# Kernel optimization log

Measured on AMD Instinct MI355X. Metric: run time of the kernel, lower is better.

The kernel has to match this reference:

```python
import jax, jax.numpy as jnp
import numpy as np

B, N, F, A, E, D, V, L = 128, 36, 2048, 1024, 1024, 1024, 10000, 20


def setup_inputs() -> dict:
    key = jax.random.key(0)
    ks = jax.random.split(key, 24)
    s = 0.02
    image_features = jax.random.normal(ks[0], (B, N, F), jnp.float32)
    encoded_captions = jax.random.randint(ks[1], (B, L), 0, V, jnp.int32)
    caption_lengths = jax.random.randint(ks[2], (B, 1), 5, L + 1, jnp.int32)
    caption_lengths = caption_lengths.at[0, 0].set(L)  # ensure max decode len = L-1
    p = lambda k, shape: jax.random.normal(k, shape, jnp.float32) * s
    return {
        "image_features": image_features,
        "encoded_captions": encoded_captions,
        "caption_lengths": caption_lengths,
        "emb": jax.random.uniform(ks[3], (V, E), jnp.float32, -0.1, 0.1),
        "W1_ih": p(ks[4], (4 * D, E + F + D)),
        "W1_hh": p(ks[5], (4 * D, D)),
        "b1_ih": jnp.zeros((4 * D,), jnp.float32),
        "b1_hh": jnp.zeros((4 * D,), jnp.float32),
        "W2_ih": p(ks[6], (4 * D, F + D)),
        "W2_hh": p(ks[7], (4 * D, D)),
        "b2_ih": jnp.zeros((4 * D,), jnp.float32),
        "b2_hh": jnp.zeros((4 * D,), jnp.float32),
        "Wf": p(ks[8], (A, F)),
        "bf": jnp.zeros((A,), jnp.float32),
        "Wd": p(ks[9], (A, D)),
        "bd": jnp.zeros((A,), jnp.float32),
        "Wa": p(ks[10], (1, A)),
        "ba": jnp.zeros((1,), jnp.float32),
        "Wfc": jax.random.uniform(ks[11], (V, D), jnp.float32, -0.1, 0.1),
        "bfc": jnp.zeros((V,), jnp.float32),
    }


def _lstm_cell(x, h, c, Wih, Whh, bih, bhh):
    g = x @ Wih.T + bih + h @ Whh.T + bhh
    i, f, gg, o = jnp.split(g, 4, axis=-1)
    c2 = jax.nn.sigmoid(f) * c + jax.nn.sigmoid(i) * jnp.tanh(gg)
    h2 = jax.nn.sigmoid(o) * jnp.tanh(c2)
    return h2, c2


def reference(image_features, encoded_captions, caption_lengths, emb,
              W1_ih, W1_hh, b1_ih, b1_hh, W2_ih, W2_hh, b2_ih, b2_hh,
              Wf, bf, Wd, bd, Wa, ba, Wfc, bfc):
    lengths = caption_lengths[:, 0]
    sort_ind = jnp.argsort(-lengths)  # descending, as in torch sort
    feats = image_features[sort_ind]            # [B,N,F]
    caps = encoded_captions[sort_ind]           # [B,L]
    dec_len = lengths[sort_ind] - 1             # [B]
    feats_mean = feats.mean(axis=1)             # [B,F]
    embs = emb[caps]                            # [B,L,E]
    att1 = feats @ Wf.T + bf                    # [B,N,A] (constant per step)
    T = caps.shape[1] - 1
    d = feats.dtype
    h1 = jnp.zeros((caps.shape[0], W1_hh.shape[1]), d)
    c1, h2, c2 = h1, h1, h1

    def step(carry, xs):
        h1, c1, h2, c2 = carry
        emb_t, t = xs
        active = (t < dec_len)[:, None].astype(d)  # ragged batch mask
        x1 = jnp.concatenate([h2, feats_mean, emb_t], axis=1)
        nh1, nc1 = _lstm_cell(x1, h1, c1, W1_ih, W1_hh, b1_ih, b1_hh)
        h1 = active * nh1 + (1.0 - active) * h1
        c1 = active * nc1 + (1.0 - active) * c1
        # additive attention (dropout is identity at eval)
        att2 = h1 @ Wd.T + bd                   # [B,A]
        e = (jax.nn.relu(att1 + att2[:, None, :]) @ Wa.T + ba)[..., 0]  # [B,N]
        alpha = jax.nn.softmax(e, axis=1)
        awe = jnp.einsum('bnf,bn->bf', feats, alpha)
        x2 = jnp.concatenate([awe, h1], axis=1)
        nh2, nc2 = _lstm_cell(x2, h2, c2, W2_ih, W2_hh, b2_ih, b2_hh)
        h2 = active * nh2 + (1.0 - active) * h2
        c2 = active * nc2 + (1.0 - active) * c2
        preds = (h2 @ Wfc.T + bfc) * active     # zeros past decode_length
        return (h1, c1, h2, c2), preds

    xs = (jnp.swapaxes(embs[:, :T, :], 0, 1), jnp.arange(T))
    _, preds = jax.lax.scan(step, (h1, c1, h2, c2), xs)
    return jnp.transpose(preds, (1, 0, 2))      # [B,T,V]
```

## Files before the change

kernel.cpp:

```cpp
#include <hip/hip_runtime.h>
#include <hip/hip_bf16.h>
#include <math.h>

#define B   128
#define NN  36
#define FF  2048
#define AA  1024
#define EE  1024
#define DD  1024
#define VV  10000
#define LL  20
#define TT  19

typedef __attribute__((ext_vector_type(8))) short short8;
typedef __attribute__((ext_vector_type(4))) float floatx4;

__global__ __launch_bounds__(B) void sort_kernel(const int* __restrict__ cap_len,
                                                 int* __restrict__ sort_ind,
                                                 int* __restrict__ dec_len) {
    __shared__ int lsh[B];
    int i = threadIdx.x;
    lsh[i] = cap_len[i];
    __syncthreads();
    int li = lsh[i];
    int rank = 0;
    for (int j = 0; j < B; ++j) {
        int lj = lsh[j];
        rank += (lj > li) || (lj == li && j < i);
    }
    sort_ind[rank] = i;
    dec_len[rank]  = li - 1;
}

__global__ void convert_kernel(const float* __restrict__ src,
                               __hip_bfloat16* __restrict__ dst, int n) {
    int i = blockIdx.x * 256 + threadIdx.x;
    if (i < n) dst[i] = __float2bfloat16(src[i]);
}

__global__ void pack_w1dyn_kernel(const float* __restrict__ Wih,
                                  const float* __restrict__ Whh,
                                  __hip_bfloat16* __restrict__ dst) {
    int i = blockIdx.x * 256 + threadIdx.x;
    int n = i >> 11, k = i & 2047;
    float v = (k < 1024) ? Wih[(size_t)n * 4096 + k] : Whh[(size_t)n * 1024 + (k - 1024)];
    dst[i] = __float2bfloat16(v);
}

__global__ void pack_w1fm_kernel(const float* __restrict__ Wih,
                                 __hip_bfloat16* __restrict__ dst) {
    int i = blockIdx.x * 256 + threadIdx.x;
    int n = i >> 11, k = i & 2047;
    dst[i] = __float2bfloat16(Wih[(size_t)n * 4096 + 1024 + k]);
}

__global__ void pack_w1emb_kernel(const float* __restrict__ Wih,
                                  __hip_bfloat16* __restrict__ dst) {
    int i = blockIdx.x * 256 + threadIdx.x;
    int n = i >> 10, k = i & 1023;
    dst[i] = __float2bfloat16(Wih[(size_t)n * 4096 + 3072 + k]);
}

__global__ void pack_w2_kernel(const float* __restrict__ Wih,
                               const float* __restrict__ Whh,
                               __hip_bfloat16* __restrict__ dst) {
    int i = blockIdx.x * 256 + threadIdx.x;
    int n = i >> 12, k = i & 4095;
    float v = (k < 3072) ? Wih[(size_t)n * 3072 + k] : Whh[(size_t)n * 1024 + (k - 3072)];
    dst[i] = __float2bfloat16(v);
}

__global__ void feats_bf_kernel(const float* __restrict__ img,
                                const int* __restrict__ sort_ind,
                                __hip_bfloat16* __restrict__ dst) {
    int i = blockIdx.x * 256 + threadIdx.x;
    int b = i / (NN * FF);
    int r = i % (NN * FF);
    dst[i] = __float2bfloat16(img[(size_t)sort_ind[b] * (NN * FF) + r]);
}

__global__ void fm_kernel(const float* __restrict__ img,
                          const int* __restrict__ sort_ind,
                          __hip_bfloat16* __restrict__ fmbf) {
    int i = blockIdx.x * 256 + threadIdx.x;
    int b = i >> 11;
    int f = i & 2047;
    const float* src = img + (size_t)sort_ind[b] * (NN * FF) + f;
    float s = 0.f;
#pragma unroll
    for (int n = 0; n < NN; ++n) s += src[n * FF];
    fmbf[i] = __float2bfloat16(s * (1.0f / NN));
}

__global__ void embcat_kernel(const float* __restrict__ emb,
                              const int* __restrict__ caps,
                              const int* __restrict__ sort_ind,
                              __hip_bfloat16* __restrict__ embcat) {
    int i = blockIdx.x * 256 + threadIdx.x;
    int row = i >> 10;
    int e = i & 1023;
    int t = row >> 7;
    int b = row & 127;
    int cap = caps[sort_ind[b] * LL + t];
    embcat[i] = __float2bfloat16(emb[(size_t)cap * EE + e]);
}

#define BM 128
#define BN 64
#define BK 64
#define LDS_K 72

template<int EPI>
__device__ __forceinline__ void gemm_core(
        short (*As)[LDS_K], short (*Wsm)[LDS_K],
        int bm, int bn, int k0,
        const __hip_bfloat16* __restrict__ A, int lda,
        const __hip_bfloat16* __restrict__ W, int ldw,
        float* __restrict__ C, int ldc,
        int N, int Kc,
        const float* __restrict__ bias,
        const int* __restrict__ dec_len) {
    const int tid  = threadIdx.x;
    const int lane = tid & 63;
    const int wv   = tid >> 6;
    const int quad = lane >> 4;
    const int l15  = lane & 15;
    const int wm   = (wv >> 1) * 64;
    const int wn   = (wv & 1) * 32;
    const int srow = tid >> 3;
    const int scol = (tid & 7) * 8;

    floatx4 acc[4][2];
#pragma unroll
    for (int i = 0; i < 4; ++i)
#pragma unroll
        for (int j = 0; j < 2; ++j)
            acc[i][j] = (floatx4){0.f, 0.f, 0.f, 0.f};

    const __hip_bfloat16* Aptr = A + (size_t)(bm + srow) * lda + k0 + scol;
    const __hip_bfloat16* Wptr = W + k0 + scol;

    for (int kt = 0; kt < Kc; kt += BK) {
#pragma unroll
        for (int p = 0; p < 4; ++p) {
            floatx4 v = *(const floatx4*)(Aptr + (size_t)(p * 32) * lda + kt);
            *(floatx4*)(&As[p * 32 + srow][scol]) = v;
        }
#pragma unroll
        for (int p = 0; p < 2; ++p) {
            int gw = bn + p * 32 + srow;
            floatx4 v;
            if (EPI != 3 || gw < N)
                v = *(const floatx4*)(Wptr + (size_t)gw * ldw + kt);
            else
                v = (floatx4){0.f, 0.f, 0.f, 0.f};
            *(floatx4*)(&Wsm[p * 32 + srow][scol]) = v;
        }
        __syncthreads();
#pragma unroll
        for (int ks = 0; ks < 2; ++ks) {
            short8 af[4], bw[2];
#pragma unroll
            for (int i = 0; i < 4; ++i)
                af[i] = *(const short8*)(&As[wm + i * 16 + l15][ks * 32 + quad * 8]);
#pragma unroll
            for (int j = 0; j < 2; ++j)
                bw[j] = *(const short8*)(&Wsm[wn + j * 16 + l15][ks * 32 + quad * 8]);
#pragma unroll
            for (int i = 0; i < 4; ++i)
#pragma unroll
                for (int j = 0; j < 2; ++j)
                    acc[i][j] = __builtin_amdgcn_mfma_f32_16x16x32_bf16(
                        af[i], bw[j], acc[i][j], 0, 0, 0);
        }
        __syncthreads();
    }

#pragma unroll
    for (int i = 0; i < 4; ++i) {
        int m = bm + wm + i * 16 + quad * 4;
#pragma unroll
        for (int j = 0; j < 2; ++j) {
            int n = bn + wn + j * 16 + l15;
            if (EPI == 3 && n >= N) continue;
#pragma unroll
            for (int r = 0; r < 4; ++r) {
                float v = acc[i][j][r];
                if (EPI == 3) {
                    int row = m + r;
                    int tt = row >> 7;
                    int bb = row & 127;
                    bool act = tt < dec_len[bb];
                    C[(size_t)bb * (TT * VV) + (size_t)tt * VV + n] =
                        act ? (v + bias[n]) : 0.f;
                } else if (EPI == 2) {
                    ((__hip_bfloat16*)C)[(size_t)(m + r) * ldc + n] = __float2bfloat16(v);
                } else {
                    C[(size_t)(m + r) * ldc + n] = v;
                }
            }
        }
    }
}

template<int EPI>
__global__ __launch_bounds__(256) void gemm_bf16(
        const __hip_bfloat16* __restrict__ A, int lda,
        const __hip_bfloat16* __restrict__ W, int ldw,
        float* __restrict__ C, int ldc, size_t pstride,
        int N, int Kc,
        const float* __restrict__ bias,
        const int* __restrict__ dec_len) {
    __shared__ __align__(16) short As[BM][LDS_K];
    __shared__ __align__(16) short Wsm[BN][LDS_K];
    gemm_core<EPI>(As, Wsm, blockIdx.y * BM, blockIdx.x * BN, blockIdx.z * Kc,
                   A, lda, W, ldw, C + (size_t)blockIdx.z * pstride, ldc,
                   N, Kc, bias, dec_len);
}

__global__ __launch_bounds__(256) void gemm_d3(
        const __hip_bfloat16* __restrict__ x2full,
        const __hip_bfloat16* __restrict__ Wd_bf,
        const __hip_bfloat16* __restrict__ W2cat,
        float* __restrict__ att2_part, size_t astride,
        float* __restrict__ g_part, size_t gstride) {
    __shared__ __align__(16) short As[BM][LDS_K];
    __shared__ __align__(16) short Wsm[BN][LDS_K];
    int idx = blockIdx.x;
    if (idx < 128) {
        int bx = idx & 15, z = idx >> 4;
        gemm_core<0>(As, Wsm, 0, bx * BN, z * 128,
                     x2full + 2048, 4096, Wd_bf, DD,
                     att2_part + (size_t)z * astride, AA,
                     AA, 128, nullptr, nullptr);
    } else {
        int j = idx - 128;
        int bx = j & 63, z = j >> 6;
        gemm_core<0>(As, Wsm, 0, bx * BN, 2048 + z * 512,
                     x2full, 4096, W2cat, 4096,
                     g_part + (size_t)(4 + z) * gstride, 4096,
                     4096, 512, nullptr, nullptr);
    }
}

template<int NZ>
__global__ void lstm_kernel(const float* __restrict__ gpart, size_t pstride,
                            const float* __restrict__ bih, const float* __restrict__ bhh,
                            const float* __restrict__ pre0, const float* __restrict__ pre1,
                            float* __restrict__ c,
                            __hip_bfloat16* __restrict__ hs1, int st1,
                            __hip_bfloat16* __restrict__ hs2, int st2,
                            __hip_bfloat16* __restrict__ hs3,
                            const int* __restrict__ dec_len, int t) {
    int idx = blockIdx.x * 256 + threadIdx.x;
    int b = idx >> 10;
    int d = idx & 1023;
    if (t >= dec_len[b]) return;
    float g[4];
#pragma unroll
    for (int gate = 0; gate < 4; ++gate) {
        size_t o = (size_t)b * 4096 + gate * 1024 + d;
        float s = bih[gate * 1024 + d] + bhh[gate * 1024 + d];
        if (pre0) s += pre0[o];
        if (pre1) s += pre1[o];
#pragma unroll
        for (int z = 0; z < NZ; ++z) s += gpart[z * pstride + o];
        g[gate] = s;
    }
    float si = 1.f / (1.f + expf(-g[0]));
    float sf = 1.f / (1.f + expf(-g[1]));
    float so = 1.f / (1.f + expf(-g[3]));
    float cc = sf * c[idx] + si * tanhf(g[2]);
    float hh = so * tanhf(cc);
    c[idx] = cc;
    __hip_bfloat16 hb = __float2bfloat16(hh);
    hs1[(size_t)b * st1 + d] = hb;
    hs2[(size_t)b * st2 + d] = hb;
    if (hs3) hs3[(size_t)b * 1024 + d] = hb;
}

__global__ __launch_bounds__(256) void att_fused(
        const float* __restrict__ p, size_t pstride,
        const float* __restrict__ bf_,
        const float* __restrict__ bd_,
        float* __restrict__ av_g,
        const __hip_bfloat16* __restrict__ att1,
        const float* __restrict__ Wa,
        const __hip_bfloat16* __restrict__ feats,
        __hip_bfloat16* __restrict__ x2full) {
    int b = blockIdx.x;
    int tid = threadIdx.x;
    __shared__ float esh[NN];
    __shared__ float alpha[NN];

#pragma unroll
    for (int rep = 0; rep < 4; ++rep) {
        int a = rep * 256 + tid;
        size_t o = (size_t)b * AA + a;
        float s = bf_[a] + bd_[a];
#pragma unroll
        for (int z = 0; z < 8; ++z) s += p[z * pstride + o];
        av_g[o] = s;
    }
    __syncthreads();

    int wv = tid >> 6, lane = tid & 63;
    const float* avp = av_g + (size_t)b * AA + lane * 16;
    const float* wap = Wa + lane * 16;
    for (int n = wv; n < NN; n += 4) {
        const __hip_bfloat16* a1 = att1 + ((size_t)b * NN + n) * AA + lane * 16;
        float pacc = 0.f;
#pragma unroll
        for (int h = 0; h < 2; ++h) {
            short8 a8 = *(const short8*)(a1 + h * 8);
            floatx4 v0 = *(const floatx4*)(avp + h * 8);
            floatx4 v1 = *(const floatx4*)(avp + h * 8 + 4);
            floatx4 w0 = *(const floatx4*)(wap + h * 8);
            floatx4 w1 = *(const floatx4*)(wap + h * 8 + 4);
            float af[8];
#pragma unroll
            for (int q = 0; q < 8; ++q) {
                union { short s; __hip_bfloat16 b; } u; u.s = a8[q];
                af[q] = __bfloat162float(u.b);
            }
#pragma unroll
            for (int q = 0; q < 4; ++q) {
                pacc += fmaxf(af[q] + v0[q], 0.f) * w0[q];
                pacc += fmaxf(af[4 + q] + v1[q], 0.f) * w1[q];
            }
        }
        for (int off = 32; off; off >>= 1) pacc += __shfl_down(pacc, off);
        if (lane == 0) esh[n] = pacc;
    }
    __syncthreads();

    if (tid < 64) {
        float ev = (tid < NN) ? esh[tid] : -INFINITY;
        float m = ev;
        for (int off = 32; off; off >>= 1) m = fmaxf(m, __shfl_down(m, off));
        m = __shfl(m, 0);
        float ex = (tid < NN) ? expf(ev - m) : 0.f;
        float s = ex;
        for (int off = 32; off; off >>= 1) s += __shfl_down(s, off);
        s = __shfl(s, 0);
        if (tid < NN) alpha[tid] = ex / s;
    }
    __syncthreads();

    const __hip_bfloat16* src = feats + (size_t)b * (NN * FF) + tid * 8;
    float s[8] = {0.f, 0.f, 0.f, 0.f, 0.f, 0.f, 0.f, 0.f};
#pragma unroll
    for (int n = 0; n < NN; ++n) {
        short8 v = *(const short8*)(src + (size_t)n * FF);
        float al = alpha[n];
#pragma unroll
        for (int q = 0; q < 8; ++q) {
            union { short s_; __hip_bfloat16 b_; } u; u.s_ = v[q];
            s[q] += al * __bfloat162float(u.b_);
        }
    }
    short8 o8;
#pragma unroll
    for (int q = 0; q < 8; ++q) {
        union { short s_; __hip_bfloat16 b_; } u; u.b_ = __float2bfloat16(s[q]);
        o8[q] = u.s_;
    }
    *(short8*)(x2full + (size_t)b * 4096 + tid * 8) = o8;
}

extern "C" void kernel_launch(void* const* d_in, const int* in_sizes, int n_in,
                              void* d_out, int out_size, void* d_ws, size_t ws_size,
                              hipStream_t stream) {
    const float* img     = (const float*)d_in[0];
    const int*   caps    = (const int*)d_in[1];
    const int*   cap_len = (const int*)d_in[2];
    const float* emb     = (const float*)d_in[3];
    const float* W1_ih   = (const float*)d_in[4];
    const float* W1_hh   = (const float*)d_in[5];
    const float* b1_ih   = (const float*)d_in[6];
    const float* b1_hh   = (const float*)d_in[7];
    const float* W2_ih   = (const float*)d_in[8];
    const float* W2_hh   = (const float*)d_in[9];
    const float* b2_ih   = (const float*)d_in[10];
    const float* b2_hh   = (const float*)d_in[11];
    const float* Wf      = (const float*)d_in[12];
    const float* bf      = (const float*)d_in[13];
    const float* Wd      = (const float*)d_in[14];
    const float* bd      = (const float*)d_in[15];
    const float* Wa      = (const float*)d_in[16];
    const float* Wfc     = (const float*)d_in[18];
    const float* bfc     = (const float*)d_in[19];
    float* out = (float*)d_out;
    (void)in_sizes; (void)n_in; (void)out_size; (void)ws_size;

    char* ws = (char*)d_ws;
    size_t off = 0;
    auto alloc = [&](size_t bytes) -> void* {
        void* p = ws + off;
        off += (bytes + 255) & ~(size_t)255;
        return p;
    };
    int* sort_ind = (int*)alloc(B * sizeof(int));
    int* dec_len  = (int*)alloc(B * sizeof(int));
    __hip_bfloat16* W1dyn    = (__hip_bfloat16*)alloc((size_t)4096 * 2048 * 2);
    __hip_bfloat16* W1fm     = (__hip_bfloat16*)alloc((size_t)4096 * 2048 * 2);
    __hip_bfloat16* W1emb    = (__hip_bfloat16*)alloc((size_t)4096 * 1024 * 2);
    __hip_bfloat16* W2cat    = (__hip_bfloat16*)alloc((size_t)4096 * 4096 * 2);
    __hip_bfloat16* Wd_bf    = (__hip_bfloat16*)alloc((size_t)AA * DD * 2);
    __hip_bfloat16* Wfc_bf   = (__hip_bfloat16*)alloc((size_t)VV * DD * 2);
    __hip_bfloat16* Wf_bf    = (__hip_bfloat16*)alloc((size_t)AA * FF * 2);
    __hip_bfloat16* feats_bf = (__hip_bfloat16*)alloc((size_t)B * NN * FF * 2);
    __hip_bfloat16* att1_bf  = (__hip_bfloat16*)alloc((size_t)B * NN * AA * 2);
    __hip_bfloat16* fmbf     = (__hip_bfloat16*)alloc((size_t)B * 2048 * 2);
    __hip_bfloat16* embcat   = (__hip_bfloat16*)alloc((size_t)TT * B * EE * 2);
    __hip_bfloat16* h2hist   = (__hip_bfloat16*)alloc((size_t)TT * B * DD * 2);
    float* gpre_fm   = (float*)alloc((size_t)B * 4096 * 4);
    float* gpre_emb  = (float*)alloc((size_t)TT * B * 4096 * 4);
    float* g_part    = (float*)alloc((size_t)8 * B * 4096 * 4);
    float* att2_part = (float*)alloc((size_t)8 * B * AA * 4);
    float* av        = (float*)alloc((size_t)B * AA * 4);
    __hip_bfloat16* x1dyn  = (__hip_bfloat16*)alloc((size_t)B * 2048 * 2);
    __hip_bfloat16* x2full = (__hip_bfloat16*)alloc((size_t)B * 4096 * 2);
    float* c1 = (float*)alloc((size_t)B * DD * 4);
    float* c2 = (float*)alloc((size_t)B * DD * 4);

    const size_t gstride = (size_t)B * 4096;
    const size_t astride = (size_t)B * AA;

    sort_kernel<<<1, B, 0, stream>>>(cap_len, sort_ind, dec_len);
    pack_w1dyn_kernel<<<(4096 * 2048) / 256, 256, 0, stream>>>(W1_ih, W1_hh, W1dyn);
    pack_w1fm_kernel<<<(4096 * 2048) / 256, 256, 0, stream>>>(W1_ih, W1fm);
    pack_w1emb_kernel<<<(4096 * 1024) / 256, 256, 0, stream>>>(W1_ih, W1emb);
    pack_w2_kernel<<<(4096 * 4096) / 256, 256, 0, stream>>>(W2_ih, W2_hh, W2cat);
    convert_kernel<<<(AA * DD) / 256, 256, 0, stream>>>(Wd, Wd_bf, AA * DD);
    convert_kernel<<<(VV * DD + 255) / 256, 256, 0, stream>>>(Wfc, Wfc_bf, VV * DD);
    convert_kernel<<<(AA * FF) / 256, 256, 0, stream>>>(Wf, Wf_bf, AA * FF);
    feats_bf_kernel<<<(B * NN * FF) / 256, 256, 0, stream>>>(img, sort_ind, feats_bf);
    fm_kernel<<<(B * 2048) / 256, 256, 0, stream>>>(img, sort_ind, fmbf);
    embcat_kernel<<<(TT * B * EE) / 256, 256, 0, stream>>>(emb, caps, sort_ind, embcat);
    hipMemsetAsync(x1dyn, 0, (size_t)B * 2048 * 2, stream);
    hipMemsetAsync(x2full, 0, (size_t)B * 4096 * 2, stream);
    hipMemsetAsync(c1, 0, (size_t)B * DD * 4, stream);
    hipMemsetAsync(c2, 0, (size_t)B * DD * 4, stream);
    hipMemsetAsync(h2hist, 0, (size_t)TT * B * DD * 2, stream);

    gemm_bf16<2><<<dim3(AA / BN, (B * NN) / BM, 1), 256, 0, stream>>>(
        feats_bf, FF, Wf_bf, FF, (float*)att1_bf, AA, 0, AA, FF, nullptr, nullptr);
    gemm_bf16<0><<<dim3(4096 / BN, 1, 1), 256, 0, stream>>>(
        fmbf, 2048, W1fm, 2048, gpre_fm, 4096, 0, 4096, 2048, nullptr, nullptr);
    gemm_bf16<0><<<dim3(4096 / BN, TT, 1), 256, 0, stream>>>(
        embcat, EE, W1emb, EE, gpre_emb, 4096, 0, 4096, EE, nullptr, nullptr);

    for (int t = 0; t < TT; ++t) {
        gemm_bf16<0><<<dim3(4096 / BN, 1, 4), 256, 0, stream>>>(
            x1dyn, 2048, W1dyn, 2048, g_part, 4096, gstride, 4096, 512,
            nullptr, nullptr);

        lstm_kernel<4><<<(B * DD) / 256, 256, 0, stream>>>(
            g_part, gstride, b1_ih, b1_hh,
            gpre_fm, gpre_emb + (size_t)t * B * 4096, c1,
            x1dyn + 1024, 2048, x2full + 2048, 4096, nullptr, dec_len, t);

        gemm_d3<<<128 + 256, 256, 0, stream>>>(
            x2full, Wd_bf, W2cat, att2_part, astride, g_part, gstride);

        att_fused<<<B, 256, 0, stream>>>(att2_part, astride, bf, bd, av,
                                         att1_bf, Wa, feats_bf, x2full);

        gemm_bf16<0><<<dim3(4096 / BN, 1, 4), 256, 0, stream>>>(
            x2full, 4096, W2cat, 4096, g_part, 4096, gstride, 4096, 512,
            nullptr, nullptr);

        lstm_kernel<8><<<(B * DD) / 256, 256, 0, stream>>>(
            g_part, gstride, b2_ih, b2_hh, nullptr, nullptr, c2,
            x1dyn + 0, 2048, x2full + 3072, 4096,
            h2hist + (size_t)t * B * DD, dec_len, t);
    }

    gemm_bf16<3><<<dim3((VV + BN - 1) / BN, TT, 1), 256, 0, stream>>>(
        h2hist, DD, Wfc_bf, DD, out, TT * VV, 0, VV, DD, bfc, dec_len);
}
```

Measured before the change: 1.696 ms.

## Merge weight packing kernels, widen attention blocks, pad vocab GEMM grid

The eight separate conversion and packing launches become one large pack_all kernel that dispatches on a global index, cutting launch count. att_fused now runs 1024 threads per batch row instead of 256, with each thread handling two feature columns rather than eight, giving more parallelism inside the serial per-step attention. The output GEMM grid is fixed at 160 column blocks, with an early-exit guard for blocks past N. The wider attention blocks give each thread less work and use narrower loads, and the fused pack kernel relies on hard-coded offset constants.

Result: faster. 1.602 ms (-5.5%).

```diff
diff --git a/kernel.cpp b/kernel.cpp
--- a/kernel.cpp
+++ b/kernel.cpp
@@ -32,51 +32,45 @@
     dec_len[rank]  = li - 1;
 }
 
-__global__ void convert_kernel(const float* __restrict__ src,
-                               __hip_bfloat16* __restrict__ dst, int n) {
-    int i = blockIdx.x * 256 + threadIdx.x;
-    if (i < n) dst[i] = __float2bfloat16(src[i]);
-}
-
-__global__ void pack_w1dyn_kernel(const float* __restrict__ Wih,
-                                  const float* __restrict__ Whh,
-                                  __hip_bfloat16* __restrict__ dst) {
-    int i = blockIdx.x * 256 + threadIdx.x;
-    int n = i >> 11, k = i & 2047;
-    float v = (k < 1024) ? Wih[(size_t)n * 4096 + k] : Whh[(size_t)n * 1024 + (k - 1024)];
-    dst[i] = __float2bfloat16(v);
-}
-
-__global__ void pack_w1fm_kernel(const float* __restrict__ Wih,
-                                 __hip_bfloat16* __restrict__ dst) {
-    int i = blockIdx.x * 256 + threadIdx.x;
-    int n = i >> 11, k = i & 2047;
-    dst[i] = __float2bfloat16(Wih[(size_t)n * 4096 + 1024 + k]);
-}
-
-__global__ void pack_w1emb_kernel(const float* __restrict__ Wih,
-                                  __hip_bfloat16* __restrict__ dst) {
-    int i = blockIdx.x * 256 + threadIdx.x;
-    int n = i >> 10, k = i & 1023;
-    dst[i] = __float2bfloat16(Wih[(size_t)n * 4096 + 3072 + k]);
-}
-
-__global__ void pack_w2_kernel(const float* __restrict__ Wih,
-                               const float* __restrict__ Whh,
-                               __hip_bfloat16* __restrict__ dst) {
-    int i = blockIdx.x * 256 + threadIdx.x;
-    int n = i >> 12, k = i & 4095;
-    float v = (k < 3072) ? Wih[(size_t)n * 3072 + k] : Whh[(size_t)n * 1024 + (k - 3072)];
-    dst[i] = __float2bfloat16(v);
-}
-
-__global__ void feats_bf_kernel(const float* __restrict__ img,
+__global__ void pack_all_kernel(const float* __restrict__ W1_ih, const float* __restrict__ W1_hh,
+                                const float* __restrict__ W2_ih, const float* __restrict__ W2_hh,
+                                const float* __restrict__ Wd,    const float* __restrict__ Wfc,
+                                const float* __restrict__ Wf,    const float* __restrict__ img,
                                 const int* __restrict__ sort_ind,
-                                __hip_bfloat16* __restrict__ dst) {
-    int i = blockIdx.x * 256 + threadIdx.x;
-    int b = i / (NN * FF);
-    int r = i % (NN * FF);
-    dst[i] = __float2bfloat16(img[(size_t)sort_ind[b] * (NN * FF) + r]);
+                                __hip_bfloat16* __restrict__ W1dyn, __hip_bfloat16* __restrict__ W1fm,
+                                __hip_bfloat16* __restrict__ W1emb, __hip_bfloat16* __restrict__ W2cat,
+                                __hip_bfloat16* __restrict__ Wd_bf, __hip_bfloat16* __restrict__ Wfc_bf,
+                                __hip_bfloat16* __restrict__ Wf_bf, __hip_bfloat16* __restrict__ feats_bf) {
+    size_t idx = (size_t)blockIdx.x * 256 + threadIdx.x;
+    if (idx < 8388608UL) {
+        size_t i = idx; int n = i >> 11, k = i & 2047;
+        float v = (k < 1024) ? W1_ih[(size_t)n * 4096 + k] : W1_hh[(size_t)n * 1024 + (k - 1024)];
+        W1dyn[i] = __float2bfloat16(v);
+    } else if (idx < 16777216UL) {
+        size_t i = idx - 8388608UL; int n = i >> 11, k = i & 2047;
+        W1fm[i] = __float2bfloat16(W1_ih[(size_t)n * 4096 + 1024 + k]);
+    } else if (idx < 20971520UL) {
+        size_t i = idx - 16777216UL; int n = i >> 10, k = i & 1023;
+        W1emb[i] = __float2bfloat16(W1_ih[(size_t)n * 4096 + 3072 + k]);
+    } else if (idx < 37748736UL) {
+        size_t i = idx - 20971520UL; int n = i >> 12, k = i & 4095;
+        float v = (k < 3072) ? W2_ih[(size_t)n * 3072 + k] : W2_hh[(size_t)n * 1024 + (k - 3072)];
+        W2cat[i] = __float2bfloat16(v);
+    } else if (idx < 38797312UL) {
+        size_t i = idx - 37748736UL;
+        Wd_bf[i] = __float2bfloat16(Wd[i]);
+    } else if (idx < 49037312UL) {
+        size_t i = idx - 38797312UL;
+        Wfc_bf[i] = __float2bfloat16(Wfc[i]);
+    } else if (idx < 51134464UL) {
+        size_t i = idx - 49037312UL;
+        Wf_bf[i] = __float2bfloat16(Wf[i]);
+    } else {
+        size_t i = idx - 51134464UL;
+        int b = (int)(i / (NN * FF));
+        int r = (int)(i % (NN * FF));
+        feats_bf[i] = __float2bfloat16(img[(size_t)sort_ind[b] * (NN * FF) + r]);
+    }
 }
 
 __global__ void fm_kernel(const float* __restrict__ img,
@@ -211,6 +205,7 @@
         int N, int Kc,
         const float* __restrict__ bias,
         const int* __restrict__ dec_len) {
+    if (blockIdx.x * BN >= N) return;
     __shared__ __align__(16) short As[BM][LDS_K];
     __shared__ __align__(16) short Wsm[BN][LDS_K];
     gemm_core<EPI>(As, Wsm, blockIdx.y * BM, blockIdx.x * BN, blockIdx.z * Kc,
@@ -279,7 +274,7 @@
     if (hs3) hs3[(size_t)b * 1024 + d] = hb;
 }
 
-__global__ __launch_bounds__(256) void att_fused(
+__global__ __launch_bounds__(1024) void att_fused(
         const float* __restrict__ p, size_t pstride,
         const float* __restrict__ bf_,
         const float* __restrict__ bd_,
@@ -293,11 +288,9 @@
     __shared__ float esh[NN];
     __shared__ float alpha[NN];
 
-#pragma unroll
-    for (int rep = 0; rep < 4; ++rep) {
-        int a = rep * 256 + tid;
-        size_t o = (size_t)b * AA + a;
-        float s = bf_[a] + bd_[a];
+    {
+        size_t o = (size_t)b * AA + tid;
+        float s = bf_[tid] + bd_[tid];
 #pragma unroll
         for (int z = 0; z < 8; ++z) s += p[z * pstride + o];
         av_g[o] = s;
@@ -307,7 +300,7 @@
     int wv = tid >> 6, lane = tid & 63;
     const float* avp = av_g + (size_t)b * AA + lane * 16;
     const float* wap = Wa + lane * 16;
-    for (int n = wv; n < NN; n += 4) {
+    for (int n = wv; n < NN; n += 16) {
         const __hip_bfloat16* a1 = att1 + ((size_t)b * NN + n) * AA + lane * 16;
         float pacc = 0.f;
 #pragma unroll
@@ -347,25 +340,20 @@
     }
     __syncthreads();
 
-    const __hip_bfloat16* src = feats + (size_t)b * (NN * FF) + tid * 8;
-    float s[8] = {0.f, 0.f, 0.f, 0.f, 0.f, 0.f, 0.f, 0.f};
+    int f0 = tid * 2;
+    const __hip_bfloat16* src = feats + (size_t)b * (NN * FF) + f0;
+    float s0 = 0.f, s1 = 0.f;
 #pragma unroll
     for (int n = 0; n < NN; ++n) {
-        short8 v = *(const short8*)(src + (size_t)n * FF);
+        __hip_bfloat162 v = *(const __hip_bfloat162*)(src + n * FF);
         float al = alpha[n];
-#pragma unroll
-        for (int q = 0; q < 8; ++q) {
-            union { short s_; __hip_bfloat16 b_; } u; u.s_ = v[q];
-            s[q] += al * __bfloat162float(u.b_);
-        }
-    }
-    short8 o8;
-#pragma unroll
-    for (int q = 0; q < 8; ++q) {
-        union { short s_; __hip_bfloat16 b_; } u; u.b_ = __float2bfloat16(s[q]);
-        o8[q] = u.s_;
-    }
-    *(short8*)(x2full + (size_t)b * 4096 + tid * 8) = o8;
+        s0 += al * __bfloat162float(v.x);
+        s1 += al * __bfloat162float(v.y);
+    }
+    __hip_bfloat162 o;
+    o.x = __float2bfloat16(s0);
+    o.y = __float2bfloat16(s1);
+    *(__hip_bfloat162*)(x2full + (size_t)b * 4096 + f0) = o;
 }
 
 extern "C" void kernel_launch(void* const* d_in, const int* in_sizes, int n_in,
@@ -428,14 +416,9 @@
     const size_t astride = (size_t)B * AA;
 
     sort_kernel<<<1, B, 0, stream>>>(cap_len, sort_ind, dec_len);
-    pack_w1dyn_kernel<<<(4096 * 2048) / 256, 256, 0, stream>>>(W1_ih, W1_hh, W1dyn);
-    pack_w1fm_kernel<<<(4096 * 2048) / 256, 256, 0, stream>>>(W1_ih, W1fm);
-    pack_w1emb_kernel<<<(4096 * 1024) / 256, 256, 0, stream>>>(W1_ih, W1emb);
-    pack_w2_kernel<<<(4096 * 4096) / 256, 256, 0, stream>>>(W2_ih, W2_hh, W2cat);
-    convert_kernel<<<(AA * DD) / 256, 256, 0, stream>>>(Wd, Wd_bf, AA * DD);
-    convert_kernel<<<(VV * DD + 255) / 256, 256, 0, stream>>>(Wfc, Wfc_bf, VV * DD);
-    convert_kernel<<<(AA * FF) / 256, 256, 0, stream>>>(Wf, Wf_bf, AA * FF);
-    feats_bf_kernel<<<(B * NN * FF) / 256, 256, 0, stream>>>(img, sort_ind, feats_bf);
+    pack_all_kernel<<<236608, 256, 0, stream>>>(
+        W1_ih, W1_hh, W2_ih, W2_hh, Wd, Wfc, Wf, img, sort_ind,
+        W1dyn, W1fm, W1emb, W2cat, Wd_bf, Wfc_bf, Wf_bf, feats_bf);
     fm_kernel<<<(B * 2048) / 256, 256, 0, stream>>>(img, sort_ind, fmbf);
     embcat_kernel<<<(TT * B * EE) / 256, 256, 0, stream>>>(emb, caps, sort_ind, embcat);
     hipMemsetAsync(x1dyn, 0, (size_t)B * 2048 * 2, stream);
@@ -464,8 +447,8 @@
         gemm_d3<<<128 + 256, 256, 0, stream>>>(
             x2full, Wd_bf, W2cat, att2_part, astride, g_part, gstride);
 
-        att_fused<<<B, 256, 0, stream>>>(att2_part, astride, bf, bd, av,
-                                         att1_bf, Wa, feats_bf, x2full);
+        att_fused<<<B, 1024, 0, stream>>>(att2_part, astride, bf, bd, av,
+                                          att1_bf, Wa, feats_bf, x2full);
 
         gemm_bf16<0><<<dim3(4096 / BN, 1, 4), 256, 0, stream>>>(
             x2full, 4096, W2cat, 4096, g_part, 4096, gstride, 4096, 512,
@@ -477,6 +460,6 @@
             h2hist + (size_t)t * B * DD, dec_len, t);
     }
 
-    gemm_bf16<3><<<dim3((VV + BN - 1) / BN, TT, 1), 256, 0, stream>>>(
+    gemm_bf16<3><<<dim3(160, TT, 1), 256, 0, stream>>>(
         h2hist, DD, Wfc_bf, DD, out, TT * VV, 0, VV, DD, bfc, dec_len);
 }
```
